# Kernel tuning notes

Hardware: AMD Instinct MI355X
Metric: run time of the kernel (lower is better)

The kernel has to match this reference:

```python
import jax, jax.numpy as jnp
import numpy as np


def _euclidean_cdist(x, q):
    # torch.cdist with p=2: pairwise L2 distances, shape [B, Q]
    x2 = jnp.sum(x * x, axis=-1, keepdims=True)          # [B, 1]
    q2 = jnp.sum(q * q, axis=-1)[None, :]                # [1, Q]
    d2 = x2 + q2 - 2.0 * (x @ q.T)                        # [B, Q]
    return jnp.sqrt(jnp.maximum(d2, 0.0))


def setup_inputs() -> dict:
    key = jax.random.key(0)
    k1, k2 = jax.random.split(key)
    x = jax.random.normal(k1, (1024, 256), dtype=jnp.float32)
    queue = jax.random.normal(k2, (32768, 256), dtype=jnp.float32)
    return {"x": x, "queue": queue}


def reference(x, queue):
    # Queue update: concat then keep the newest max_size rows (queue assumed full)
    max_size = queue.shape[0]
    q = jnp.concatenate([queue, x], axis=0)[-max_size:]   # [Q, F]
    # Distance matrix + top-2 nearest (topk of negated distances)
    d = _euclidean_cdist(x, q)                            # [B, Q]
    _, idx = jax.lax.top_k(-d, 2)                         # [B, 2]
    # Second-nearest neighbor (first is the point itself, dist 0)
    return q[idx[:, 1]]                                   # [B, F]
```

## Files before the change

kernel.cpp:

```cpp
#include <hip/hip_runtime.h>
#include <stdint.h>

#define B_ROWS 1024
#define FEAT   256
#define QSZ    32768
#define SHIFT  1024
#define QX     (QSZ - B_ROWS)
#define NQB    256
#define NXB    8
#define MARGIN 8.0f

typedef float  v4f __attribute__((ext_vector_type(4)));
typedef short  v8s __attribute__((ext_vector_type(8)));

__device__ __forceinline__ uint32_t key_flip(uint32_t u) {
    return u ^ ((uint32_t)((int32_t)u >> 31) | 0x80000000u);
}
__device__ __forceinline__ float key_m(uint32_t k) {
    uint32_t u = k & 0xFFFF8000u;
    u = (u & 0x80000000u) ? (u ^ 0x80000000u) : ~u;
    return __uint_as_float(u);
}
__device__ __forceinline__ void k2_insert(uint32_t& k1, uint32_t& k2, uint32_t key) {
    uint32_t hi = max(k1, key); k1 = min(k1, key); k2 = min(k2, hi);
}
__device__ __forceinline__ uint2 k2_merge(uint2 a, uint2 b) {
    uint32_t hi = max(a.x, b.x);
    uint2 r; r.x = min(a.x, b.x); r.y = min(min(a.y, b.y), hi);
    return r;
}

struct Top2 { float m1; int j1; float m2; int j2; };
__device__ __forceinline__ bool better(float ma, int ja, float mb, int jb) {
    return (ma < mb) || (ma == mb && ja < jb);
}
__device__ __forceinline__ void t2_insert(Top2& t, float m, int j) {
    if (better(m, j, t.m1, t.j1)) { t.m2 = t.m1; t.j2 = t.j1; t.m1 = m; t.j1 = j; }
    else if (better(m, j, t.m2, t.j2)) { t.m2 = m; t.j2 = j; }
}

__device__ __forceinline__ const float* q_row_ptr(int j, const float* x, const float* queue) {
    return (j < QX) ? (queue + (size_t)(j + SHIFT) * FEAT) : (x + (size_t)(j - QX) * FEAT);
}

__device__ __forceinline__ unsigned short f2bf(float f) {
    uint32_t u = __float_as_uint(f);
    uint32_t r = u + 0x7FFFu + ((u >> 16) & 1u);
    return (unsigned short)(r >> 16);
}

__device__ __forceinline__ void lds_load16(const void* g, void* l) {
    __builtin_amdgcn_global_load_lds(
        (const __attribute__((address_space(1))) uint32_t*)g,
        (__attribute__((address_space(3))) uint32_t*)l, 16, 0, 0);
}

__global__ __launch_bounds__(256) void convert_kernel(const float* __restrict__ x,
                                                      const float* __restrict__ queue,
                                                      unsigned short* __restrict__ q_bf,
                                                      float* __restrict__ q2) {
    int wave = threadIdx.x >> 6, lane = threadIdx.x & 63;
    int j = blockIdx.x * 4 + wave;
    const float4* row = (const float4*)q_row_ptr(j, x, queue);
    float4 v = row[lane];
    float s = v.x * v.x + v.y * v.y + v.z * v.z + v.w * v.w;
#pragma unroll
    for (int off = 32; off; off >>= 1) s += __shfl_xor(s, off, 64);
    if (lane == 0) q2[j] = s;
    ushort4 h;
    h.x = f2bf(v.x); h.y = f2bf(v.y); h.z = f2bf(v.z); h.w = f2bf(v.w);
    ((ushort4*)q_bf)[(size_t)j * 64 + lane] = h;
}

__device__ __forceinline__ void stage_chunk(const unsigned short* gA, const unsigned short* gB,
                                            unsigned short* asb, unsigned short* bsb,
                                            int w, int c) {
    lds_load16(gA + (size_t)c * 32,             asb + (w * 32) * 32);
    lds_load16(gA + (size_t)c * 32 + 16 * FEAT, asb + (w * 32 + 16) * 32);
    lds_load16(gB + (size_t)c * 32,             bsb + (w * 32) * 32);
    lds_load16(gB + (size_t)c * 32 + 16 * FEAT, bsb + (w * 32 + 16) * 32);
}

__global__ __launch_bounds__(256, 3) void nn_mfma(const unsigned short* __restrict__ q_bf,
                                                  const float* __restrict__ q2,
                                                  uint2* __restrict__ partials) {
    __shared__ unsigned short As[2][128 * 32];
    __shared__ unsigned short Bs[2][128 * 32];
    __shared__ uint2 scr[128][2];

    const int t    = threadIdx.x;
    const int w    = t >> 6, lane = t & 63;
    const int wm   = w >> 1, wn = w & 1;
    const int quad = lane >> 4, l16 = lane & 15;

    const int p  = blockIdx.x;
    const int gy = (p & 7) * 32 + (p >> 6);
    const int gx = (p >> 3) & 7;

    const unsigned short* x_bf = q_bf + (size_t)QX * FEAT;

    const int srow = lane >> 2;
    const int sgl  = (lane & 3) ^ ((lane >> 3) & 3);
    const unsigned short* gA = q_bf + (size_t)(gy * 128 + w * 32 + srow) * FEAT + sgl * 8;
    const unsigned short* gB = x_bf + (size_t)(gx * 128 + w * 32 + srow) * FEAT + sgl * 8;

    v4f acc[4][4];
#pragma unroll
    for (int a = 0; a < 4; ++a)
#pragma unroll
        for (int b = 0; b < 4; ++b) acc[a][b] = (v4f)0.0f;

    const int gphys = quad ^ ((l16 >> 1) & 3);
    const char* Ard = (const char*)&As[0][0] + (size_t)(wm * 64 + l16) * 64 + gphys * 16;
    const char* Brd = (const char*)&Bs[0][0] + (size_t)(wn * 64 + l16) * 64 + gphys * 16;

    stage_chunk(gA, gB, As[0], Bs[0], w, 0);

#pragma unroll
    for (int c = 0; c < 8; ++c) {
        if (c < 7) stage_chunk(gA, gB, As[(c + 1) & 1], Bs[(c + 1) & 1], w, c + 1);
        __builtin_amdgcn_sched_barrier(0);
        if (c < 7) asm volatile("s_waitcnt vmcnt(4)" ::: "memory");
        else       asm volatile("s_waitcnt vmcnt(0)" ::: "memory");
        __builtin_amdgcn_s_barrier();

        const char* Ac = Ard + (c & 1) * 8192;
        const char* Bc = Brd + (c & 1) * 8192;
        v8s fa[4], fb[4];
#pragma unroll
        for (int tm = 0; tm < 4; ++tm) fa[tm] = *(const v8s*)(Ac + tm * 1024);
#pragma unroll
        for (int tn = 0; tn < 4; ++tn) fb[tn] = *(const v8s*)(Bc + tn * 1024);
        __builtin_amdgcn_s_setprio(1);
#pragma unroll
        for (int tm = 0; tm < 4; ++tm)
#pragma unroll
            for (int tn = 0; tn < 4; ++tn)
                acc[tm][tn] = __builtin_amdgcn_mfma_f32_16x16x32_bf16(fa[tm], fb[tn], acc[tm][tn], 0, 0, 0);
        __builtin_amdgcn_s_setprio(0);
        __builtin_amdgcn_s_barrier();
    }

    float q2r[4][4];
#pragma unroll
    for (int tm = 0; tm < 4; ++tm) {
        v4f qq = *(const v4f*)(q2 + gy * 128 + wm * 64 + tm * 16 + quad * 4);
#pragma unroll
        for (int r = 0; r < 4; ++r) q2r[tm][r] = qq[r];
    }
    const int jbase = gy * 128 + wm * 64 + quad * 4;

    uint2 best[4];
#pragma unroll
    for (int tn = 0; tn < 4; ++tn) {
        uint32_t k1 = 0xFFFFFFFFu, k2 = 0xFFFFFFFFu;
#pragma unroll
        for (int tm = 0; tm < 4; ++tm)
#pragma unroll
            for (int r = 0; r < 4; ++r) {
                float m = fmaf(-2.0f, acc[tm][tn][r], q2r[tm][r]);
                uint32_t u = key_flip(__float_as_uint(m));
                uint32_t key = (u & 0xFFFF8000u) | (uint32_t)(jbase + tm * 16 + r);
                k2_insert(k1, k2, key);
            }
#pragma unroll
        for (int mask = 16; mask <= 32; mask <<= 1) {
            uint32_t o1 = __shfl_xor(k1, mask, 64);
            uint32_t o2 = __shfl_xor(k2, mask, 64);
            uint32_t hi = max(k1, o1);
            k1 = min(k1, o1);
            k2 = min(min(k2, o2), hi);
        }
        best[tn] = make_uint2(k1, k2);
    }
    if (quad == 0) {
#pragma unroll
        for (int tn = 0; tn < 4; ++tn) scr[wn * 64 + tn * 16 + l16][wm] = best[tn];
    }
    __syncthreads();
    if (t < 128) {
        uint2 r = k2_merge(scr[t][0], scr[t][1]);
        partials[(size_t)(gx * 128 + t) * NQB + gy] = r;
    }
}

__global__ __launch_bounds__(256) void nn_finalize(const float* __restrict__ x,
                                                   const float* __restrict__ queue,
                                                   const float* __restrict__ q2,
                                                   const uint2* __restrict__ partials,
                                                   float* __restrict__ out) {
    __shared__ float    xs[256];
    __shared__ uint2    red[256];
    __shared__ int      list[64];
    __shared__ float    escore[64];
    __shared__ int      s_cnt;
    __shared__ uint32_t s_kcut;
    __shared__ int      s_j2;

    const int t = threadIdx.x, i = blockIdx.x;
    const int w = t >> 6, lane = t & 63;

    xs[t] = x[(size_t)i * FEAT + t];
    uint2 p = partials[(size_t)i * NQB + t];
    red[t] = p;
    if (t == 0) s_cnt = 0;
    __syncthreads();

    if (w == 0) {
        uint2 a = red[lane];
        a = k2_merge(a, red[lane + 64]);
        a = k2_merge(a, red[lane + 128]);
        a = k2_merge(a, red[lane + 192]);
#pragma unroll
        for (int mask = 1; mask <= 32; mask <<= 1) {
            uint2 o;
            o.x = __shfl_xor(a.x, mask, 64);
            o.y = __shfl_xor(a.y, mask, 64);
            a = k2_merge(a, o);
        }
        if (lane == 0) {
            float cutf = key_m(a.y) + MARGIN;
            s_kcut = key_flip(__float_as_uint(cutf)) | 0x7FFFu;
        }
    }
    __syncthreads();
    uint32_t kcut = s_kcut;
    if (p.x <= kcut) { int q_ = atomicAdd(&s_cnt, 1); if (q_ < 64) list[q_] = (int)(p.x & 0x7FFFu); }
    if (p.y <= kcut) { int q_ = atomicAdd(&s_cnt, 1); if (q_ < 64) list[q_] = (int)(p.y & 0x7FFFu); }
    __syncthreads();
    int n = min(s_cnt, 64);

    for (int c = w; c < n; c += 4) {
        int j = list[c];
        const float4* qr = (const float4*)q_row_ptr(j, x, queue);
        float4 qv = qr[lane];
        float4 xv = ((const float4*)xs)[lane];
        float s = qv.x * xv.x + qv.y * xv.y + qv.z * xv.z + qv.w * xv.w;
#pragma unroll
        for (int off = 32; off; off >>= 1) s += __shfl_xor(s, off, 64);
        if (lane == 0) escore[c] = q2[j] - 2.0f * s;
    }
    __syncthreads();
    if (t == 0) {
        Top2 a;
        a.m1 = __builtin_inff(); a.j1 = 0x7FFFFFFF;
        a.m2 = __builtin_inff(); a.j2 = 0x7FFFFFFF;
        for (int c = 0; c < n; ++c) t2_insert(a, escore[c], list[c]);
        s_j2 = a.j2;
    }
    __syncthreads();
    out[(size_t)i * FEAT + t] = q_row_ptr(s_j2, x, queue)[t];
}

extern "C" void kernel_launch(void* const* d_in, const int* in_sizes, int n_in,
                              void* d_out, int out_size, void* d_ws, size_t ws_size,
                              hipStream_t stream) {
    const float* x     = (const float*)d_in[0];
    const float* queue = (const float*)d_in[1];

    unsigned short* q_bf     = (unsigned short*)d_ws;
    float*          q2       = (float*)((char*)d_ws + (16u << 20));
    uint2*          partials = (uint2*)((char*)d_ws + (17u << 20));

    convert_kernel<<<QSZ / 4, 256, 0, stream>>>(x, queue, q_bf, q2);
    nn_mfma<<<NQB * NXB, 256, 0, stream>>>(q_bf, q2, partials);
    nn_finalize<<<B_ROWS, 256, 0, stream>>>(x, queue, q2, partials, (float*)d_out);
}
```

Before: 111.4 us.

## Fuse queue bf16 conversion and norms into MFMA distance kernel

The separate conversion pass over the whole 32K-row queue is removed. Each block now loads its 64 queue rows in fp32, converts them to bf16 into a swizzled LDS tile held for the block's lifetime, and computes their squared norms. It then streams all 1024 x rows through double-buffered LDS to produce partial top-2 results. This avoids writing and re-reading the 16MB bf16 queue copy, at the cost of a smaller M tile, more blocks, and finalize merging 512 partials per row instead of 256.

```diff
diff --git a/kernel.cpp b/kernel.cpp
--- a/kernel.cpp
+++ b/kernel.cpp
@@ -6,8 +6,8 @@
 #define QSZ    32768
 #define SHIFT  1024
 #define QX     (QSZ - B_ROWS)
-#define NQB    256
-#define NXB    8
+#define BM     64
+#define NGY    (QSZ / BM)
 #define MARGIN 8.0f
 
 typedef float  v4f __attribute__((ext_vector_type(4)));
@@ -55,132 +55,137 @@
         (__attribute__((address_space(3))) uint32_t*)l, 16, 0, 0);
 }
 
-__global__ __launch_bounds__(256) void convert_kernel(const float* __restrict__ x,
-                                                      const float* __restrict__ queue,
-                                                      unsigned short* __restrict__ q_bf,
-                                                      float* __restrict__ q2) {
+__global__ __launch_bounds__(256) void convert_x(const float* __restrict__ x,
+                                                 unsigned short* __restrict__ x_bf) {
     int wave = threadIdx.x >> 6, lane = threadIdx.x & 63;
-    int j = blockIdx.x * 4 + wave;
-    const float4* row = (const float4*)q_row_ptr(j, x, queue);
-    float4 v = row[lane];
-    float s = v.x * v.x + v.y * v.y + v.z * v.z + v.w * v.w;
-#pragma unroll
-    for (int off = 32; off; off >>= 1) s += __shfl_xor(s, off, 64);
-    if (lane == 0) q2[j] = s;
+    int r = blockIdx.x * 4 + wave;
+    float4 v = ((const float4*)(x + (size_t)r * FEAT))[lane];
     ushort4 h;
     h.x = f2bf(v.x); h.y = f2bf(v.y); h.z = f2bf(v.z); h.w = f2bf(v.w);
-    ((ushort4*)q_bf)[(size_t)j * 64 + lane] = h;
-}
-
-__device__ __forceinline__ void stage_chunk(const unsigned short* gA, const unsigned short* gB,
-                                            unsigned short* asb, unsigned short* bsb,
-                                            int w, int c) {
-    lds_load16(gA + (size_t)c * 32,             asb + (w * 32) * 32);
-    lds_load16(gA + (size_t)c * 32 + 16 * FEAT, asb + (w * 32 + 16) * 32);
-    lds_load16(gB + (size_t)c * 32,             bsb + (w * 32) * 32);
-    lds_load16(gB + (size_t)c * 32 + 16 * FEAT, bsb + (w * 32 + 16) * 32);
-}
-
-__global__ __launch_bounds__(256, 3) void nn_mfma(const unsigned short* __restrict__ q_bf,
-                                                  const float* __restrict__ q2,
-                                                  uint2* __restrict__ partials) {
-    __shared__ unsigned short As[2][128 * 32];
-    __shared__ unsigned short Bs[2][128 * 32];
-    __shared__ uint2 scr[128][2];
+    ((ushort4*)x_bf)[(size_t)r * 64 + lane] = h;
+}
+
+__global__ __launch_bounds__(256, 3) void nn_fused(const float* __restrict__ x,
+                                                   const float* __restrict__ queue,
+                                                   const unsigned short* __restrict__ x_bf,
+                                                   float* __restrict__ q2,
+                                                   uint2* __restrict__ partials) {
+    __shared__ __align__(16) unsigned short As[BM * FEAT];
+    __shared__ __align__(16) unsigned short Bs[2][128 * 32];
+    __shared__ __align__(16) float sq2[BM];
 
     const int t    = threadIdx.x;
     const int w    = t >> 6, lane = t & 63;
-    const int wm   = w >> 1, wn = w & 1;
     const int quad = lane >> 4, l16 = lane & 15;
-
-    const int p  = blockIdx.x;
-    const int gy = (p & 7) * 32 + (p >> 6);
-    const int gx = (p >> 3) & 7;
-
-    const unsigned short* x_bf = q_bf + (size_t)QX * FEAT;
+    const int gy   = blockIdx.x;
 
     const int srow = lane >> 2;
     const int sgl  = (lane & 3) ^ ((lane >> 3) & 3);
-    const unsigned short* gA = q_bf + (size_t)(gy * 128 + w * 32 + srow) * FEAT + sgl * 8;
-    const unsigned short* gB = x_bf + (size_t)(gx * 128 + w * 32 + srow) * FEAT + sgl * 8;
-
-    v4f acc[4][4];
+    const unsigned short* gB0 = x_bf + (size_t)(w * 32 + srow) * FEAT + sgl * 8;
+    lds_load16(gB0,             &Bs[0][(w * 32) * 32]);
+    lds_load16(gB0 + 16 * FEAT, &Bs[0][(w * 32 + 16) * 32]);
+
+    const int arow = t >> 2, aqtr = t & 3;
+    const float* asrc = q_row_ptr(gy * BM + arow, x, queue) + aqtr * 64;
+    float ss = 0.0f;
+#pragma unroll
+    for (int gi = 0; gi < 8; ++gi) {
+        float4 a = *(const float4*)(asrc + gi * 8);
+        float4 b = *(const float4*)(asrc + gi * 8 + 4);
+        ss += a.x * a.x + a.y * a.y + a.z * a.z + a.w * a.w
+            + b.x * b.x + b.y * b.y + b.z * b.z + b.w * b.w;
+        uint32_t p0 = (uint32_t)f2bf(a.x) | ((uint32_t)f2bf(a.y) << 16);
+        uint32_t p1 = (uint32_t)f2bf(a.z) | ((uint32_t)f2bf(a.w) << 16);
+        uint32_t p2 = (uint32_t)f2bf(b.x) | ((uint32_t)f2bf(b.y) << 16);
+        uint32_t p3 = (uint32_t)f2bf(b.z) | ((uint32_t)f2bf(b.w) << 16);
+        const int g    = aqtr * 8 + gi;
+        const int phys = (g & 24) | ((g & 7) ^ (arow & 7));
+        *(uint4*)&As[arow * FEAT + phys * 8] = make_uint4(p0, p1, p2, p3);
+    }
+    ss += __shfl_xor(ss, 1, 64);
+    ss += __shfl_xor(ss, 2, 64);
+    if (aqtr == 0) { sq2[arow] = ss; q2[gy * BM + arow] = ss; }
+
+    v4f acc[4][2];
 #pragma unroll
     for (int a = 0; a < 4; ++a)
 #pragma unroll
-        for (int b = 0; b < 4; ++b) acc[a][b] = (v4f)0.0f;
-
-    const int gphys = quad ^ ((l16 >> 1) & 3);
-    const char* Ard = (const char*)&As[0][0] + (size_t)(wm * 64 + l16) * 64 + gphys * 16;
-    const char* Brd = (const char*)&Bs[0][0] + (size_t)(wn * 64 + l16) * 64 + gphys * 16;
-
-    stage_chunk(gA, gB, As[0], Bs[0], w, 0);
-
-#pragma unroll
-    for (int c = 0; c < 8; ++c) {
-        if (c < 7) stage_chunk(gA, gB, As[(c + 1) & 1], Bs[(c + 1) & 1], w, c + 1);
-        __builtin_amdgcn_sched_barrier(0);
-        if (c < 7) asm volatile("s_waitcnt vmcnt(4)" ::: "memory");
-        else       asm volatile("s_waitcnt vmcnt(0)" ::: "memory");
-        __builtin_amdgcn_s_barrier();
-
-        const char* Ac = Ard + (c & 1) * 8192;
-        const char* Bc = Brd + (c & 1) * 8192;
-        v8s fa[4], fb[4];
-#pragma unroll
-        for (int tm = 0; tm < 4; ++tm) fa[tm] = *(const v8s*)(Ac + tm * 1024);
-#pragma unroll
-        for (int tn = 0; tn < 4; ++tn) fb[tn] = *(const v8s*)(Bc + tn * 1024);
-        __builtin_amdgcn_s_setprio(1);
-#pragma unroll
-        for (int tm = 0; tm < 4; ++tm)
-#pragma unroll
-            for (int tn = 0; tn < 4; ++tn)
-                acc[tm][tn] = __builtin_amdgcn_mfma_f32_16x16x32_bf16(fa[tm], fb[tn], acc[tm][tn], 0, 0, 0);
-        __builtin_amdgcn_s_setprio(0);
-        __builtin_amdgcn_s_barrier();
-    }
-
-    float q2r[4][4];
-#pragma unroll
-    for (int tm = 0; tm < 4; ++tm) {
-        v4f qq = *(const v4f*)(q2 + gy * 128 + wm * 64 + tm * 16 + quad * 4);
-#pragma unroll
-        for (int r = 0; r < 4; ++r) q2r[tm][r] = qq[r];
-    }
-    const int jbase = gy * 128 + wm * 64 + quad * 4;
-
-    uint2 best[4];
-#pragma unroll
-    for (int tn = 0; tn < 4; ++tn) {
-        uint32_t k1 = 0xFFFFFFFFu, k2 = 0xFFFFFFFFu;
-#pragma unroll
-        for (int tm = 0; tm < 4; ++tm)
-#pragma unroll
-            for (int r = 0; r < 4; ++r) {
-                float m = fmaf(-2.0f, acc[tm][tn][r], q2r[tm][r]);
-                uint32_t u = key_flip(__float_as_uint(m));
-                uint32_t key = (u & 0xFFFF8000u) | (uint32_t)(jbase + tm * 16 + r);
-                k2_insert(k1, k2, key);
+        for (int b = 0; b < 2; ++b) acc[a][b] = (v4f)0.0f;
+
+    const int  gphysB = quad ^ ((l16 >> 1) & 3);
+    const char* Brd = (const char*)&Bs[0][0] + (size_t)(w * 32 + l16) * 64 + gphysB * 16;
+
+    __syncthreads();
+
+    for (int gx = 0; gx < 8; ++gx) {
+#pragma unroll
+        for (int c = 0; c < 8; ++c) {
+            const int m = gx * 8 + c;
+            if (m < 63) {
+                const int mm = m + 1;
+                const unsigned short* gBn = gB0 + (size_t)(mm >> 3) * (128 * FEAT) + (mm & 7) * 32;
+                unsigned short* dstb = &Bs[(c + 1) & 1][(w * 32) * 32];
+                lds_load16(gBn,             dstb);
+                lds_load16(gBn + 16 * FEAT, dstb + 16 * 32);
+                __builtin_amdgcn_sched_barrier(0);
+                asm volatile("s_waitcnt vmcnt(2)" ::: "memory");
+            } else {
+                __builtin_amdgcn_sched_barrier(0);
+                asm volatile("s_waitcnt vmcnt(0)" ::: "memory");
             }
-#pragma unroll
-        for (int mask = 16; mask <= 32; mask <<= 1) {
-            uint32_t o1 = __shfl_xor(k1, mask, 64);
-            uint32_t o2 = __shfl_xor(k2, mask, 64);
-            uint32_t hi = max(k1, o1);
-            k1 = min(k1, o1);
-            k2 = min(min(k2, o2), hi);
-        }
-        best[tn] = make_uint2(k1, k2);
-    }
-    if (quad == 0) {
-#pragma unroll
-        for (int tn = 0; tn < 4; ++tn) scr[wn * 64 + tn * 16 + l16][wm] = best[tn];
-    }
-    __syncthreads();
-    if (t < 128) {
-        uint2 r = k2_merge(scr[t][0], scr[t][1]);
-        partials[(size_t)(gx * 128 + t) * NQB + gy] = r;
+            __builtin_amdgcn_s_barrier();
+
+            const int physA = ((c >> 1) * 8) | ((((c & 1) * 4) + quad) ^ (l16 & 7));
+            v8s fa[4], fb[2];
+#pragma unroll
+            for (int tm = 0; tm < 4; ++tm)
+                fa[tm] = *(const v8s*)((const char*)As + (size_t)(tm * 16 + l16) * 512 + physA * 16);
+            const char* Bc = Brd + (c & 1) * 8192;
+#pragma unroll
+            for (int tn = 0; tn < 2; ++tn)
+                fb[tn] = *(const v8s*)(Bc + tn * 1024);
+            __builtin_amdgcn_s_setprio(1);
+#pragma unroll
+            for (int tm = 0; tm < 4; ++tm)
+#pragma unroll
+                for (int tn = 0; tn < 2; ++tn)
+                    acc[tm][tn] = __builtin_amdgcn_mfma_f32_16x16x32_bf16(fa[tm], fb[tn], acc[tm][tn], 0, 0, 0);
+            __builtin_amdgcn_s_setprio(0);
+            __builtin_amdgcn_s_barrier();
+        }
+
+        float q2r[4][4];
+#pragma unroll
+        for (int tm = 0; tm < 4; ++tm) {
+            v4f qq = *(const v4f*)&sq2[tm * 16 + quad * 4];
+#pragma unroll
+            for (int r = 0; r < 4; ++r) q2r[tm][r] = qq[r];
+        }
+        const int jbase = gy * BM + quad * 4;
+#pragma unroll
+        for (int tn = 0; tn < 2; ++tn) {
+            uint32_t k1 = 0xFFFFFFFFu, k2 = 0xFFFFFFFFu;
+#pragma unroll
+            for (int tm = 0; tm < 4; ++tm)
+#pragma unroll
+                for (int r = 0; r < 4; ++r) {
+                    float mv = fmaf(-2.0f, acc[tm][tn][r], q2r[tm][r]);
+                    uint32_t u = key_flip(__float_as_uint(mv));
+                    uint32_t key = (u & 0xFFFF8000u) | (uint32_t)(jbase + tm * 16 + r);
+                    k2_insert(k1, k2, key);
+                    acc[tm][tn][r] = 0.0f;
+                }
+#pragma unroll
+            for (int mask = 16; mask <= 32; mask <<= 1) {
+                uint32_t o1 = __shfl_xor(k1, mask, 64);
+                uint32_t o2 = __shfl_xor(k2, mask, 64);
+                uint32_t hi = max(k1, o1);
+                k1 = min(k1, o1);
+                k2 = min(min(k2, o2), hi);
+            }
+            if (quad == 0)
+                partials[(size_t)(gx * 128 + w * 32 + tn * 16 + l16) * NGY + gy] = make_uint2(k1, k2);
+        }
     }
 }
 
@@ -201,8 +206,10 @@
     const int w = t >> 6, lane = t & 63;
 
     xs[t] = x[(size_t)i * FEAT + t];
-    uint2 p = partials[(size_t)i * NQB + t];
-    red[t] = p;
+    uint2 pa = partials[(size_t)i * NGY + t];
+    uint2 pb = partials[(size_t)i * NGY + 256 + t];
+    uint2 pm = k2_merge(pa, pb);
+    red[t] = pm;
     if (t == 0) s_cnt = 0;
     __syncthreads();
 
@@ -225,8 +232,8 @@
     }
     __syncthreads();
     uint32_t kcut = s_kcut;
-    if (p.x <= kcut) { int q_ = atomicAdd(&s_cnt, 1); if (q_ < 64) list[q_] = (int)(p.x & 0x7FFFu); }
-    if (p.y <= kcut) { int q_ = atomicAdd(&s_cnt, 1); if (q_ < 64) list[q_] = (int)(p.y & 0x7FFFu); }
+    if (pm.x <= kcut) { int q_ = atomicAdd(&s_cnt, 1); if (q_ < 64) list[q_] = (int)(pm.x & 0x7FFFu); }
+    if (pm.y <= kcut) { int q_ = atomicAdd(&s_cnt, 1); if (q_ < 64) list[q_] = (int)(pm.y & 0x7FFFu); }
     __syncthreads();
     int n = min(s_cnt, 64);
 
@@ -258,11 +265,11 @@
     const float* x     = (const float*)d_in[0];
     const float* queue = (const float*)d_in[1];
 
-    unsigned short* q_bf     = (unsigned short*)d_ws;
-    float*          q2       = (float*)((char*)d_ws + (16u << 20));
-    uint2*          partials = (uint2*)((char*)d_ws + (17u << 20));
-
-    convert_kernel<<<QSZ / 4, 256, 0, stream>>>(x, queue, q_bf, q2);
-    nn_mfma<<<NQB * NXB, 256, 0, stream>>>(q_bf, q2, partials);
+    unsigned short* x_bf     = (unsigned short*)d_ws;
+    float*          q2       = (float*)((char*)d_ws + (1u << 20));
+    uint2*          partials = (uint2*)((char*)d_ws + (2u << 20));
+
+    convert_x<<<B_ROWS / 4, 256, 0, stream>>>(x, x_bf);
+    nn_fused<<<NGY, 256, 0, stream>>>(x, queue, x_bf, q2, partials);
     nn_finalize<<<B_ROWS, 256, 0, stream>>>(x, queue, q2, partials, (float*)d_out);
 }
```

Result: slower. 119.0 us (+6.8%).
